# Performance work log

Measured on AMD Instinct MI355X. Metric: run time of the kernel, lower is better.

The kernel has to match this reference:

```python
import jax, jax.numpy as jnp
import numpy as np

B, N, D_IN = 16, 2048, 256
C, H = 32, 64          # num_capsules, dim_capsules
HEADS, KD = 4, 64      # attention heads, key_dim = dim_capsules
ROUTINGS = 3
EPS_SQ = 1e-7
LN_EPS = 1e-3


def squash(v, axis=-1):
    s2 = jnp.sum(jnp.square(v), axis=axis, keepdims=True)
    scale = s2 / (1.0 + s2) / jnp.sqrt(s2 + EPS_SQ)
    return scale * v


def setup_inputs() -> dict:
    key = jax.random.key(0)
    ks = jax.random.split(key, 10)
    # VarianceScaling(scale=2.0, fan_avg, uniform) for W
    fan_avg = (D_IN + H) / 2.0
    limit = float(np.sqrt(3.0 * 2.0 / fan_avg))
    W = jax.random.uniform(ks[0], (C, D_IN, H), minval=-limit, maxval=limit, dtype=jnp.float32)
    b_caps = jnp.zeros((C, H), jnp.float32)
    gamma = jnp.full((1,), 3.0, jnp.float32)
    x = jax.random.normal(ks[1], (B, N, D_IN), dtype=jnp.float32)
    def glorot(k, shape):
        fin, fout = shape[0], int(np.prod(shape[1:]))
        lim = float(np.sqrt(6.0 / (fin + fout)))
        return jax.random.uniform(k, shape, minval=-lim, maxval=lim, dtype=jnp.float32)
    Wq = glorot(ks[2], (H, HEADS, KD)); bq = jnp.zeros((HEADS, KD), jnp.float32)
    Wk = glorot(ks[3], (H, HEADS, KD)); bk = jnp.zeros((HEADS, KD), jnp.float32)
    Wv = glorot(ks[4], (H, HEADS, KD)); bv = jnp.zeros((HEADS, KD), jnp.float32)
    Wo = glorot(ks[5], (HEADS, KD, H)); bo = jnp.zeros((H,), jnp.float32)
    ln_gamma = jnp.ones((H,), jnp.float32)
    ln_beta = jnp.zeros((H,), jnp.float32)
    return dict(x=x, W=W, b_caps=b_caps, gamma=gamma,
                Wq=Wq, bq=bq, Wk=Wk, bk=bk, Wv=Wv, bv=bv, Wo=Wo, bo=bo,
                ln_gamma=ln_gamma, ln_beta=ln_beta)


def dynamic_routing(u_hat):
    # u_hat: [B, N, C, H]
    b = jnp.zeros(u_hat.shape[:3] + (1,), u_hat.dtype)
    v = None
    for i in range(ROUTINGS):
        c = jax.nn.softmax(b, axis=2)                      # [B,N,C,1]
        s = jnp.sum(c * u_hat, axis=1, keepdims=True)      # [B,1,C,H]
        v = squash(s, axis=-1)
        if i < ROUTINGS - 1:
            agreement = jnp.sum(u_hat * v, axis=-1, keepdims=True)
            b = b + agreement
    return jnp.squeeze(v, axis=1)                          # [B,C,H]


def mha_self(xq, Wq, bq, Wk, bk, Wv, bv, Wo, bo):
    # xq: [B, C, H]
    q = jnp.einsum('bch,hnk->bcnk', xq, Wq) + bq
    k = jnp.einsum('bch,hnk->bcnk', xq, Wk) + bk
    v = jnp.einsum('bch,hnk->bcnk', xq, Wv) + bv
    scores = jnp.einsum('bqnd,bknd->bnqk', q, k) / jnp.sqrt(jnp.asarray(KD, xq.dtype))
    attn = jax.nn.softmax(scores, axis=-1)
    ctx = jnp.einsum('bnqk,bknd->bqnd', attn, v)
    return jnp.einsum('bqnd,ndh->bqh', ctx, Wo) + bo


def reference(x, W, b_caps, gamma, Wq, bq, Wk, bk, Wv, bv, Wo, bo, ln_gamma, ln_beta):
    u_hat = jnp.einsum('bnd,cdh->bnch', x, W) + b_caps[None, None]  # [B,N,C,H]
    routed = dynamic_routing(u_hat)                                  # [B,C,H]
    attended = mha_self(routed, Wq, bq, Wk, bk, Wv, bv, Wo, bo)
    y = attended + routed
    mu = jnp.mean(y, axis=-1, keepdims=True)
    var = jnp.mean(jnp.square(y - mu), axis=-1, keepdims=True)
    routed = (y - mu) / jnp.sqrt(var + LN_EPS) * ln_gamma + ln_beta
    return squash(routed, axis=-1) * gamma
```

## Files before the change

### kernel.cpp

```cpp
#include <hip/hip_runtime.h>
#include <cstddef>

typedef _Float16 f16;
typedef __attribute__((ext_vector_type(8))) _Float16 f16x8;
typedef __attribute__((ext_vector_type(4))) float f32x4;

namespace {
constexpr int kB = 16;
constexpr int kN = 2048;
constexpr int kD = 256;
constexpr int kC = 32;
constexpr int kH = 64;
constexpr int kHeads = 4;
constexpr int kKD = 64;
constexpr int kChunks = 32;
constexpr int kRows = kN / kChunks;
constexpr int kXJ = 64;

constexpr size_t OFF_XPART = 0;
constexpr size_t OFF_V     = OFF_XPART + 262144;
constexpr size_t OFF_WV    = OFF_V + 32768;
constexpr size_t OFF_BV    = OFF_WV + 131072;
constexpr size_t OFF_Y     = OFF_BV + 512;
constexpr size_t OFF_CS    = OFF_Y + 131072;
constexpr size_t OFF_QKV   = OFF_CS + 512;
constexpr size_t OFF_CTX   = OFF_QKV + 393216;
constexpr size_t OFF_XF16  = OFF_CTX + 524288;
constexpr size_t OFF_WVH   = OFF_XF16 + 4194304;
constexpr size_t OFF_CSP   = OFF_WVH + 65536;
constexpr size_t OFF_YP    = OFF_CSP + 16384;
constexpr size_t WS_NEED_PARTIAL = (OFF_YP + 4194304) * sizeof(float);
}

__global__ __launch_bounds__(256) void k_xpart(const float* __restrict__ x,
                                               float* __restrict__ xpart,
                                               f16* __restrict__ xh) {
  const int b = blockIdx.x, j = blockIdx.y, d = threadIdx.x;
  const size_t base = ((size_t)b * kN + (size_t)j * 32) * kD + d;
  const float* xp = x + base;
  f16* xo = xh + base;
  float s = 0.f;
#pragma unroll
  for (int n = 0; n < 32; ++n) {
    const float v = xp[(size_t)n * kD];
    s += v;
    xo[(size_t)n * kD] = (f16)v;
  }
  xpart[((size_t)b * kXJ + j) * kD + d] = s;
}

__global__ __launch_bounds__(256) void k_sv(
    const float* __restrict__ W, const float* __restrict__ b_caps,
    const float* __restrict__ xpart, const float* __restrict__ y,
    const float* __restrict__ csum, const float* __restrict__ ypart,
    const float* __restrict__ cspart, float* __restrict__ v,
    float* __restrict__ Wv, f16* __restrict__ Wvh, float* __restrict__ bv,
    const int mode, const int computeWv, const int accWv, const int npart) {
  const int bc = blockIdx.x, b = bc >> 5, c = bc & 31;
  const int t = threadIdx.x;
  const int w = t >> 6, h = t & 63;
  __shared__ float yL[kD];
  __shared__ float sL[4][kH];
  __shared__ float vL[kH];
  __shared__ float csLs;

  if (mode == 0) {
    float s = 0.f;
#pragma unroll 8
    for (int j = 0; j < kXJ; ++j) s += xpart[((size_t)b * kXJ + j) * kD + t];
    yL[t] = s * (1.f / (float)kC);
    if (t == 0) csLs = (float)kN / (float)kC;
  } else if (npart > 0) {
    float s = 0.f;
#pragma unroll 8
    for (int ch = 0; ch < kChunks; ++ch)
      s += ypart[(((size_t)b * kChunks + ch) * kC + c) * kD + t];
    yL[t] = s;
    if (t < 32) {
      float cs_ = cspart[((size_t)b * kChunks + t) * kC + c];
#pragma unroll
      for (int off = 16; off; off >>= 1) cs_ += __shfl_xor(cs_, off, 64);
      if (t == 0) csLs = cs_;
    }
  } else {
    yL[t] = y[(size_t)bc * kD + t];
    if (t == 0) csLs = csum[bc];
  }
  __syncthreads();

  const float* Wc = W + (size_t)c * kD * kH;
  {
    float acc = 0.f;
#pragma unroll 8
    for (int d = w * 64; d < (w + 1) * 64; ++d)
      acc = fmaf(yL[d], Wc[(size_t)d * kH + h], acc);
    sL[w][h] = acc;
  }
  __syncthreads();

  if (t < 64) {
    const float bch = b_caps[c * kH + h];
    float s = sL[0][h] + sL[1][h] + sL[2][h] + sL[3][h] + csLs * bch;
    float s2 = s * s;
#pragma unroll
    for (int off = 32; off; off >>= 1) s2 += __shfl_xor(s2, off, 64);
    const float scale = s2 / (1.f + s2) * rsqrtf(s2 + 1e-7f);
    const float vh = scale * s;
    v[(size_t)bc * kH + h] = vh;
    vL[h] = vh;
    if (computeWv) {
      float bvp = bch * vh;
#pragma unroll
      for (int off = 32; off; off >>= 1) bvp += __shfl_xor(bvp, off, 64);
      if (h == 0) bv[bc] = accWv ? (bv[bc] + bvp) : bvp;
    }
  }
  __syncthreads();
  if (computeWv) {
    float acc = 0.f;
    const float* Wrow = Wc + (size_t)t * kH;
#pragma unroll 8
    for (int hh = 0; hh < kH; ++hh) acc = fmaf(Wrow[hh], vL[hh], acc);
    const size_t idx = (size_t)bc * kD + t;
    const float nv = accWv ? (Wv[idx] + acc) : acc;
    Wv[idx] = nv;
    Wvh[idx] = (f16)nv;
  }
}

__global__ __launch_bounds__(256) void k_route(
    const f16* __restrict__ xh, const f16* __restrict__ Wvh,
    const float* __restrict__ bv, float* __restrict__ y,
    float* __restrict__ csum, float* __restrict__ ypart,
    float* __restrict__ cspart, const int usePart) {
  const int b = blockIdx.x, chunk = blockIdx.y;
  const int t = threadIdx.x;
  const int lane = t & 63, w = t >> 6;
  const int l15 = lane & 15, q = lane >> 4;

  __shared__ __align__(16) f16 xsT[kD][kRows + 8];
  __shared__ float aL[kRows][kC + 4];
  __shared__ __align__(16) f16 pT[kC][kRows + 8];
  __shared__ float csL[8][kC];

  const int n0 = chunk * kRows;
  const float bvc = bv[b * kC + (t & 31)];

  f32x4 acc0 = {0.f, 0.f, 0.f, 0.f}, acc1 = {0.f, 0.f, 0.f, 0.f};
  {
    const int row = w * 16 + l15;
    const f16x8* Ar = reinterpret_cast<const f16x8*>(
        xh + ((size_t)(b * kN + n0 + row)) * kD + q * 8);
    const f16x8* B0 = reinterpret_cast<const f16x8*>(
        Wvh + ((size_t)(b * kC + l15)) * kD + q * 8);
    const f16x8* B1 = reinterpret_cast<const f16x8*>(
        Wvh + ((size_t)(b * kC + 16 + l15)) * kD + q * 8);
#pragma unroll
    for (int ks = 0; ks < 8; ++ks) {
      f16x8 af = Ar[ks * 4];
      acc0 = __builtin_amdgcn_mfma_f32_16x16x32_f16(af, B0[ks * 4], acc0, 0, 0, 0);
      acc1 = __builtin_amdgcn_mfma_f32_16x16x32_f16(af, B1[ks * 4], acc1, 0, 0, 0);
      const int dbase = ks * 32 + q * 8;
#pragma unroll
      for (int i = 0; i < 8; ++i) {
        const int ii = (i + 2 * q) & 7;
        xsT[dbase + ii][row] = af[ii];
      }
    }
  }
#pragma unroll
  for (int r = 0; r < 4; ++r) {
    aL[w * 16 + q * 4 + r][l15] = acc0[r];
    aL[w * 16 + q * 4 + r][16 + l15] = acc1[r];
  }
  __syncthreads();

  const int c = t & 31, sg = t >> 5;
  float csreg = 0.f;
#pragma unroll
  for (int k = 0; k < 8; ++k) {
    const int r = sg * 8 + k;
    float L = bvc + aL[r][c];
    float m = L;
#pragma unroll
    for (int off = 16; off; off >>= 1) m = fmaxf(m, __shfl_xor(m, off, 64));
    const float e = __expf(L - m);
    float ssum = e;
#pragma unroll
    for (int off = 16; off; off >>= 1) ssum += __shfl_xor(ssum, off, 64);
    const float p = e / ssum;
    pT[c][r] = (f16)p;
    csreg += p;
  }
  csL[sg][c] = csreg;
  __syncthreads();

  const int mt2 = w & 1;
  const int ntb = (w >> 1) * 8;
  const f16x8 a0 = *reinterpret_cast<const f16x8*>(&pT[mt2 * 16 + l15][q * 8]);
  const f16x8 a1 = *reinterpret_cast<const f16x8*>(&pT[mt2 * 16 + l15][32 + q * 8]);
  const int cap = mt2 * 16 + q * 4;
#pragma unroll
  for (int i = 0; i < 8; ++i) {
    const int d0 = (ntb + i) * 16;
    const f16x8 b0 = *reinterpret_cast<const f16x8*>(&xsT[d0 + l15][q * 8]);
    const f16x8 b1 = *reinterpret_cast<const f16x8*>(&xsT[d0 + l15][32 + q * 8]);
    f32x4 o = {0.f, 0.f, 0.f, 0.f};
    o = __builtin_amdgcn_mfma_f32_16x16x32_f16(a0, b0, o, 0, 0, 0);
    o = __builtin_amdgcn_mfma_f32_16x16x32_f16(a1, b1, o, 0, 0, 0);
    if (usePart) {
      float* dst = ypart + (((size_t)(b * kChunks + chunk)) * kC + cap) * kD + d0 + l15;
#pragma unroll
      for (int r = 0; r < 4; ++r) dst[(size_t)r * kD] = o[r];
    } else {
      float* dst = y + ((size_t)(b * kC + cap)) * kD + d0 + l15;
#pragma unroll
      for (int r = 0; r < 4; ++r) atomicAdd(dst + (size_t)r * kD, o[r]);
    }
  }
  if (t < 32) {
    float s = 0.f;
#pragma unroll
    for (int j = 0; j < 8; ++j) s += csL[j][t];
    if (usePart) cspart[((size_t)b * kChunks + chunk) * kC + t] = s;
    else atomicAdd(csum + b * kC + t, s);
  }
}

__global__ __launch_bounds__(256) void k_qkv(
    const float* __restrict__ routed, const float* __restrict__ Wq,
    const float* __restrict__ bq, const float* __restrict__ Wk,
    const float* __restrict__ bk, const float* __restrict__ Wvp,
    const float* __restrict__ bvp, float* __restrict__ qkv) {
  const int b = blockIdx.x, head = blockIdx.y, which = blockIdx.z;
  const int t = threadIdx.x;
  const int kk = t & 63, w = t >> 6;
  const float* Wsrc = (which == 0) ? Wq : (which == 1) ? Wk : Wvp;
  const float* bsrc = (which == 0) ? bq : (which == 1) ? bk : bvp;
  __shared__ float rL[kC * kH];
#pragma unroll
  for (int i = 0; i < 8; ++i) rL[t + 256 * i] = routed[(size_t)b * kC * kH + t + 256 * i];
  __syncthreads();
  float acc[8];
  const float bb = bsrc[head * kKD + kk];
#pragma unroll
  for (int i = 0; i < 8; ++i) acc[i] = bb;
#pragma unroll 4
  for (int hh = 0; hh < kH; ++hh) {
    const float wv = Wsrc[((size_t)hh * kHeads + head) * kKD + kk];
#pragma unroll
    for (int i = 0; i < 8; ++i)
      acc[i] = fmaf(rL[(w + 4 * i) * kH + hh], wv, acc[i]);
  }
#pragma unroll
  for (int i = 0; i < 8; ++i) {
    const int cc = w + 4 * i;
    qkv[((((size_t)which * kB + b) * kHeads + head) * kC + cc) * kKD + kk] = acc[i];
  }
}

__global__ __launch_bounds__(256) void k_attn2(const float* __restrict__ qkv,
                                               float* __restrict__ ctx) {
  const int b = blockIdx.x, head = blockIdx.y, t = threadIdx.x;
  constexpr size_t kWhichStride = (size_t)kB * kHeads * kC * kKD;
  const size_t base = ((size_t)b * kHeads + head) * kC * kKD;
  __shared__ float qL[kC][kKD];
  __shared__ float kL[kC][kKD + 1];
  __shared__ float vL[kC][kKD];
  __shared__ float sc[kC][kC + 1];
#pragma unroll
  for (int i = 0; i < 8; ++i) {
    const int e = t + 256 * i, cc = e >> 6, kk = e & 63;
    qL[cc][kk] = qkv[base + e];
    kL[cc][kk] = qkv[base + kWhichStride + e];
    vL[cc][kk] = qkv[base + 2 * kWhichStride + e];
  }
  __syncthreads();
#pragma unroll
  for (int i = 0; i < 4; ++i) {
    const int e = t + 256 * i, qc = e >> 5, kc = e & 31;
    float s = 0.f;
#pragma unroll 8
    for (int d = 0; d < kKD; ++d) s = fmaf(qL[qc][d], kL[kc][d], s);
    sc[qc][kc] = s * 0.125f;
  }
  __syncthreads();
  if (t < kC) {
    float m = -1e30f;
#pragma unroll
    for (int kc = 0; kc < kC; ++kc) m = fmaxf(m, sc[t][kc]);
    float ssum = 0.f;
#pragma unroll
    for (int kc = 0; kc < kC; ++kc) {
      const float e2 = __expf(sc[t][kc] - m);
      sc[t][kc] = e2;
      ssum += e2;
    }
    const float inv = 1.f / ssum;
#pragma unroll
    for (int kc = 0; kc < kC; ++kc) sc[t][kc] *= inv;
  }
  __syncthreads();
#pragma unroll
  for (int i = 0; i < 8; ++i) {
    const int e = t + 256 * i, qc = e >> 6, d = e & 63;
    float s = 0.f;
#pragma unroll 8
    for (int kc = 0; kc < kC; ++kc) s = fmaf(sc[qc][kc], vL[kc][d], s);
    ctx[(((size_t)b * kC + qc) * kHeads + head) * kKD + d] = s;
  }
}

__global__ __launch_bounds__(256) void k_final(
    const float* __restrict__ ctx, const float* __restrict__ Wo,
    const float* __restrict__ bo, const float* __restrict__ routed,
    const float* __restrict__ ln_g, const float* __restrict__ ln_b,
    const float* __restrict__ gamma, float* __restrict__ out) {
  const int bc = blockIdx.x, t = threadIdx.x;
  const int w = t >> 6, h = t & 63;
  __shared__ float cL[kHeads * kKD];
  __shared__ float sL[4][kH];
  cL[t] = ctx[(size_t)bc * (kHeads * kKD) + t];
  __syncthreads();
  float acc = 0.f;
#pragma unroll 8
  for (int nd = w * 64; nd < (w + 1) * 64; ++nd)
    acc = fmaf(cL[nd], Wo[(size_t)nd * kH + h], acc);
  sL[w][h] = acc;
  __syncthreads();
  if (t < 64) {
    const float yv = sL[0][h] + sL[1][h] + sL[2][h] + sL[3][h] + bo[h] +
                     routed[(size_t)bc * kH + h];
    float mu = yv;
#pragma unroll
    for (int off = 32; off; off >>= 1) mu += __shfl_xor(mu, off, 64);
    mu *= (1.f / (float)kH);
    const float dv = yv - mu;
    float var = dv * dv;
#pragma unroll
    for (int off = 32; off; off >>= 1) var += __shfl_xor(var, off, 64);
    var *= (1.f / (float)kH);
    const float nrm = dv * rsqrtf(var + 1e-3f) * ln_g[h] + ln_b[h];
    float s2 = nrm * nrm;
#pragma unroll
    for (int off = 32; off; off >>= 1) s2 += __shfl_xor(s2, off, 64);
    const float scale = s2 / (1.f + s2) * rsqrtf(s2 + 1e-7f);
    out[(size_t)bc * kH + h] = scale * nrm * gamma[0];
  }
}

extern "C" void kernel_launch(void* const* d_in, const int* in_sizes, int n_in,
                              void* d_out, int out_size, void* d_ws, size_t ws_size,
                              hipStream_t stream) {
  (void)in_sizes; (void)n_in; (void)out_size;
  const float* x      = (const float*)d_in[0];
  const float* W      = (const float*)d_in[1];
  const float* b_caps = (const float*)d_in[2];
  const float* gamma  = (const float*)d_in[3];
  const float* Wq     = (const float*)d_in[4];
  const float* bq     = (const float*)d_in[5];
  const float* Wk     = (const float*)d_in[6];
  const float* bk     = (const float*)d_in[7];
  const float* Wv_in  = (const float*)d_in[8];
  const float* bv_in  = (const float*)d_in[9];
  const float* Wo     = (const float*)d_in[10];
  const float* bo     = (const float*)d_in[11];
  const float* ln_g   = (const float*)d_in[12];
  const float* ln_b   = (const float*)d_in[13];
  float* out = (float*)d_out;
  float* ws  = (float*)d_ws;

  float* xpart = ws + OFF_XPART;
  float* v     = ws + OFF_V;
  float* Wv    = ws + OFF_WV;
  float* bv    = ws + OFF_BV;
  float* y     = ws + OFF_Y;
  float* cs    = ws + OFF_CS;
  float* qkv   = ws + OFF_QKV;
  float* ctx   = ws + OFF_CTX;
  f16*   xf16  = (f16*)(ws + OFF_XF16);
  f16*   wvh   = (f16*)(ws + OFF_WVH);
  float* csp   = ws + OFF_CSP;
  float* yp    = ws + OFF_YP;

  const int usePart = (ws_size >= WS_NEED_PARTIAL) ? 1 : 0;

  k_xpart<<<dim3(kB, kXJ), 256, 0, stream>>>(x, xpart, xf16);
  k_sv<<<kB * kC, 256, 0, stream>>>(W, b_caps, xpart, y, cs, yp, csp, v, Wv, wvh, bv,
                                    0, 1, 0, 0);

  if (!usePart) {
    hipMemsetAsync(y, 0, (size_t)kB * kC * kD * sizeof(float), stream);
    hipMemsetAsync(cs, 0, (size_t)kB * kC * sizeof(float), stream);
  }
  k_route<<<dim3(kB, kChunks), 256, 0, stream>>>(xf16, wvh, bv, y, cs, yp, csp, usePart);
  k_sv<<<kB * kC, 256, 0, stream>>>(W, b_caps, xpart, y, cs, yp, csp, v, Wv, wvh, bv,
                                    1, 1, 1,
                                    usePart ? kChunks : 0);

  if (!usePart) {
    hipMemsetAsync(y, 0, (size_t)kB * kC * kD * sizeof(float), stream);
    hipMemsetAsync(cs, 0, (size_t)kB * kC * sizeof(float), stream);
  }
  k_route<<<dim3(kB, kChunks), 256, 0, stream>>>(xf16, wvh, bv, y, cs, yp, csp, usePart);
  k_sv<<<kB * kC, 256, 0, stream>>>(W, b_caps, xpart, y, cs, yp, csp, v, Wv, wvh, bv,
                                    1, 0, 0,
                                    usePart ? kChunks : 0);

  k_qkv<<<dim3(kB, kHeads, 3), 256, 0, stream>>>(v, Wq, bq, Wk, bk, Wv_in, bv_in, qkv);
  k_attn2<<<dim3(kB, kHeads), 256, 0, stream>>>(qkv, ctx);
  k_final<<<kB * kC, 256, 0, stream>>>(ctx, Wo, bo, v, ln_g, ln_b, gamma, out);
}
```

Baseline: 179.0 us.

## Fuse final squash, QKV, attention and output projection into one per-batch kernel

```diff
diff --git a/kernel.cpp b/kernel.cpp
--- a/kernel.cpp
+++ b/kernel.cpp
@@ -2,6 +2,7 @@
 #include <cstddef>
 
 typedef _Float16 f16;
+typedef __attribute__((ext_vector_type(4))) _Float16 f16x4;
 typedef __attribute__((ext_vector_type(8))) _Float16 f16x8;
 typedef __attribute__((ext_vector_type(4))) float f32x4;
 
@@ -23,9 +24,7 @@
 constexpr size_t OFF_BV    = OFF_WV + 131072;
 constexpr size_t OFF_Y     = OFF_BV + 512;
 constexpr size_t OFF_CS    = OFF_Y + 131072;
-constexpr size_t OFF_QKV   = OFF_CS + 512;
-constexpr size_t OFF_CTX   = OFF_QKV + 393216;
-constexpr size_t OFF_XF16  = OFF_CTX + 524288;
+constexpr size_t OFF_XF16  = OFF_CS + 512;
 constexpr size_t OFF_WVH   = OFF_XF16 + 4194304;
 constexpr size_t OFF_CSP   = OFF_WVH + 65536;
 constexpr size_t OFF_YP    = OFF_CSP + 16384;
@@ -35,18 +34,25 @@
 __global__ __launch_bounds__(256) void k_xpart(const float* __restrict__ x,
                                                float* __restrict__ xpart,
                                                f16* __restrict__ xh) {
-  const int b = blockIdx.x, j = blockIdx.y, d = threadIdx.x;
-  const size_t base = ((size_t)b * kN + (size_t)j * 32) * kD + d;
-  const float* xp = x + base;
-  f16* xo = xh + base;
-  float s = 0.f;
-#pragma unroll
-  for (int n = 0; n < 32; ++n) {
-    const float v = xp[(size_t)n * kD];
-    s += v;
-    xo[(size_t)n * kD] = (f16)v;
-  }
-  xpart[((size_t)b * kXJ + j) * kD + d] = s;
+  const int b = blockIdx.x, j = blockIdx.y;
+  const int t = threadIdx.x;
+  const int rg = t >> 6, dq = t & 63;
+  __shared__ float sL[4][kD];
+  float4 s = {0.f, 0.f, 0.f, 0.f};
+  const size_t rowbase = (size_t)b * kN + (size_t)j * 32;
+#pragma unroll
+  for (int i = 0; i < 8; ++i) {
+    const int r = rg * 8 + i;
+    const float4 q = *(reinterpret_cast<const float4*>(x + (rowbase + r) * kD) + dq);
+    s.x += q.x; s.y += q.y; s.z += q.z; s.w += q.w;
+    f16x4 h4 = {(f16)q.x, (f16)q.y, (f16)q.z, (f16)q.w};
+    *(reinterpret_cast<f16x4*>(xh + (rowbase + r) * kD) + dq) = h4;
+  }
+  reinterpret_cast<float4*>(&sL[rg][0])[dq] = s;
+  __syncthreads();
+  const int d = t;
+  xpart[((size_t)b * kXJ + j) * kD + d] =
+      sL[0][d] + sL[1][d] + sL[2][d] + sL[3][d];
 }
 
 __global__ __launch_bounds__(256) void k_sv(
@@ -227,125 +233,181 @@
   }
 }
 
-__global__ __launch_bounds__(256) void k_qkv(
-    const float* __restrict__ routed, const float* __restrict__ Wq,
-    const float* __restrict__ bq, const float* __restrict__ Wk,
-    const float* __restrict__ bk, const float* __restrict__ Wvp,
-    const float* __restrict__ bvp, float* __restrict__ qkv) {
-  const int b = blockIdx.x, head = blockIdx.y, which = blockIdx.z;
-  const int t = threadIdx.x;
-  const int kk = t & 63, w = t >> 6;
-  const float* Wsrc = (which == 0) ? Wq : (which == 1) ? Wk : Wvp;
-  const float* bsrc = (which == 0) ? bq : (which == 1) ? bk : bvp;
-  __shared__ float rL[kC * kH];
-#pragma unroll
-  for (int i = 0; i < 8; ++i) rL[t + 256 * i] = routed[(size_t)b * kC * kH + t + 256 * i];
-  __syncthreads();
-  float acc[8];
-  const float bb = bsrc[head * kKD + kk];
-#pragma unroll
-  for (int i = 0; i < 8; ++i) acc[i] = bb;
+__global__ __launch_bounds__(256) void k_tail(
+    const float* __restrict__ W, const float* __restrict__ b_caps,
+    const float* __restrict__ y, const float* __restrict__ csum,
+    const float* __restrict__ ypart, const float* __restrict__ cspart,
+    const float* __restrict__ Wq, const float* __restrict__ bq,
+    const float* __restrict__ Wk, const float* __restrict__ bk,
+    const float* __restrict__ Wvp, const float* __restrict__ bvp,
+    const float* __restrict__ Wo, const float* __restrict__ bo,
+    const float* __restrict__ ln_g, const float* __restrict__ ln_b,
+    const float* __restrict__ gamma, float* __restrict__ out,
+    const int usePart) {
+  const int b = blockIdx.x, t = threadIdx.x;
+  const int w = t >> 6, h = t & 63;
+  __shared__ float yL[kC][kD];
+  __shared__ float rL[kC][kH];
+  __shared__ float csLs[kC];
+  __shared__ float qLs[kC][kKD];
+  __shared__ float kLs[kC][kKD + 1];
+  __shared__ float vLs[kC][kKD];
+  __shared__ float scs[kC][kC + 1];
+
+  if (usePart) {
+    const int c = t >> 3, fq = t & 7;
+    float4 acc[8];
+#pragma unroll
+    for (int i = 0; i < 8; ++i) acc[i] = {0.f, 0.f, 0.f, 0.f};
+    for (int ch = 0; ch < kChunks; ++ch) {
+      const float4* src = reinterpret_cast<const float4*>(
+          ypart + (((size_t)(b * kChunks + ch)) * kC + c) * kD);
+#pragma unroll
+      for (int i = 0; i < 8; ++i) {
+        const float4 q = src[fq + 8 * i];
+        acc[i].x += q.x; acc[i].y += q.y; acc[i].z += q.z; acc[i].w += q.w;
+      }
+    }
+    float4* dst = reinterpret_cast<float4*>(&yL[c][0]);
+#pragma unroll
+    for (int i = 0; i < 8; ++i) dst[fq + 8 * i] = acc[i];
+    if (t < kC) {
+      float s = 0.f;
+      for (int ch = 0; ch < kChunks; ++ch)
+        s += cspart[((size_t)b * kChunks + ch) * kC + t];
+      csLs[t] = s;
+    }
+  } else {
+    const int c = t >> 3, fq = t & 7;
+    const float4* src = reinterpret_cast<const float4*>(y + ((size_t)(b * kC + c)) * kD);
+    float4* dst = reinterpret_cast<float4*>(&yL[c][0]);
+#pragma unroll
+    for (int i = 0; i < 8; ++i) dst[fq + 8 * i] = src[fq + 8 * i];
+    if (t < kC) csLs[t] = csum[b * kC + t];
+  }
+  __syncthreads();
+
+  {
+    float sacc[8];
+#pragma unroll
+    for (int i = 0; i < 8; ++i) {
+      const int c = w + 4 * i;
+      sacc[i] = csLs[c] * b_caps[c * kH + h];
+    }
+#pragma unroll
+    for (int i = 0; i < 8; ++i) {
+      const int c = w + 4 * i;
+      const float* Wc = W + ((size_t)c * kD) * kH + h;
+      float a = sacc[i];
+#pragma unroll 8
+      for (int d = 0; d < kD; ++d) a = fmaf(yL[c][d], Wc[(size_t)d * kH], a);
+      sacc[i] = a;
+    }
+#pragma unroll
+    for (int i = 0; i < 8; ++i) {
+      const int c = w + 4 * i;
+      float s2 = sacc[i] * sacc[i];
+#pragma unroll
+      for (int off = 32; off; off >>= 1) s2 += __shfl_xor(s2, off, 64);
+      const float scale = s2 / (1.f + s2) * rsqrtf(s2 + 1e-7f);
+      rL[c][h] = scale * sacc[i];
+    }
+  }
+  __syncthreads();
+
+  for (int head = 0; head < kHeads; ++head) {
+    float aq[8], ak[8], av[8];
+    const float bq_ = bq[head * kKD + h];
+    const float bk_ = bk[head * kKD + h];
+    const float bv_ = bvp[head * kKD + h];
+#pragma unroll
+    for (int i = 0; i < 8; ++i) { aq[i] = bq_; ak[i] = bk_; av[i] = bv_; }
 #pragma unroll 4
-  for (int hh = 0; hh < kH; ++hh) {
-    const float wv = Wsrc[((size_t)hh * kHeads + head) * kKD + kk];
-#pragma unroll
-    for (int i = 0; i < 8; ++i)
-      acc[i] = fmaf(rL[(w + 4 * i) * kH + hh], wv, acc[i]);
-  }
-#pragma unroll
-  for (int i = 0; i < 8; ++i) {
-    const int cc = w + 4 * i;
-    qkv[((((size_t)which * kB + b) * kHeads + head) * kC + cc) * kKD + kk] = acc[i];
-  }
-}
-
-__global__ __launch_bounds__(256) void k_attn2(const float* __restrict__ qkv,
-                                               float* __restrict__ ctx) {
-  const int b = blockIdx.x, head = blockIdx.y, t = threadIdx.x;
-  constexpr size_t kWhichStride = (size_t)kB * kHeads * kC * kKD;
-  const size_t base = ((size_t)b * kHeads + head) * kC * kKD;
-  __shared__ float qL[kC][kKD];
-  __shared__ float kL[kC][kKD + 1];
-  __shared__ float vL[kC][kKD];
-  __shared__ float sc[kC][kC + 1];
-#pragma unroll
-  for (int i = 0; i < 8; ++i) {
-    const int e = t + 256 * i, cc = e >> 6, kk = e & 63;
-    qL[cc][kk] = qkv[base + e];
-    kL[cc][kk] = qkv[base + kWhichStride + e];
-    vL[cc][kk] = qkv[base + 2 * kWhichStride + e];
-  }
-  __syncthreads();
-#pragma unroll
-  for (int i = 0; i < 4; ++i) {
-    const int e = t + 256 * i, qc = e >> 5, kc = e & 31;
-    float s = 0.f;
-#pragma unroll 8
-    for (int d = 0; d < kKD; ++d) s = fmaf(qL[qc][d], kL[kc][d], s);
-    sc[qc][kc] = s * 0.125f;
-  }
-  __syncthreads();
-  if (t < kC) {
-    float m = -1e30f;
-#pragma unroll
-    for (int kc = 0; kc < kC; ++kc) m = fmaxf(m, sc[t][kc]);
-    float ssum = 0.f;
-#pragma unroll
-    for (int kc = 0; kc < kC; ++kc) {
-      const float e2 = __expf(sc[t][kc] - m);
-      sc[t][kc] = e2;
-      ssum += e2;
-    }
-    const float inv = 1.f / ssum;
-#pragma unroll
-    for (int kc = 0; kc < kC; ++kc) sc[t][kc] *= inv;
-  }
-  __syncthreads();
-#pragma unroll
-  for (int i = 0; i < 8; ++i) {
-    const int e = t + 256 * i, qc = e >> 6, d = e & 63;
-    float s = 0.f;
-#pragma unroll 8
-    for (int kc = 0; kc < kC; ++kc) s = fmaf(sc[qc][kc], vL[kc][d], s);
-    ctx[(((size_t)b * kC + qc) * kHeads + head) * kKD + d] = s;
-  }
-}
-
-__global__ __launch_bounds__(256) void k_final(
-    const float* __restrict__ ctx, const float* __restrict__ Wo,
-    const float* __restrict__ bo, const float* __restrict__ routed,
-    const float* __restrict__ ln_g, const float* __restrict__ ln_b,
-    const float* __restrict__ gamma, float* __restrict__ out) {
-  const int bc = blockIdx.x, t = threadIdx.x;
-  const int w = t >> 6, h = t & 63;
-  __shared__ float cL[kHeads * kKD];
-  __shared__ float sL[4][kH];
-  cL[t] = ctx[(size_t)bc * (kHeads * kKD) + t];
-  __syncthreads();
-  float acc = 0.f;
-#pragma unroll 8
-  for (int nd = w * 64; nd < (w + 1) * 64; ++nd)
-    acc = fmaf(cL[nd], Wo[(size_t)nd * kH + h], acc);
-  sL[w][h] = acc;
-  __syncthreads();
-  if (t < 64) {
-    const float yv = sL[0][h] + sL[1][h] + sL[2][h] + sL[3][h] + bo[h] +
-                     routed[(size_t)bc * kH + h];
-    float mu = yv;
-#pragma unroll
-    for (int off = 32; off; off >>= 1) mu += __shfl_xor(mu, off, 64);
-    mu *= (1.f / (float)kH);
-    const float dv = yv - mu;
-    float var = dv * dv;
-#pragma unroll
-    for (int off = 32; off; off >>= 1) var += __shfl_xor(var, off, 64);
-    var *= (1.f / (float)kH);
-    const float nrm = dv * rsqrtf(var + 1e-3f) * ln_g[h] + ln_b[h];
-    float s2 = nrm * nrm;
-#pragma unroll
-    for (int off = 32; off; off >>= 1) s2 += __shfl_xor(s2, off, 64);
-    const float scale = s2 / (1.f + s2) * rsqrtf(s2 + 1e-7f);
-    out[(size_t)bc * kH + h] = scale * nrm * gamma[0];
+    for (int hh = 0; hh < kH; ++hh) {
+      const size_t wi = ((size_t)hh * kHeads + head) * kKD + h;
+      const float wq = Wq[wi], wk = Wk[wi], wv2 = Wvp[wi];
+#pragma unroll
+      for (int i = 0; i < 8; ++i) {
+        const float r = rL[w + 4 * i][hh];
+        aq[i] = fmaf(r, wq, aq[i]);
+        ak[i] = fmaf(r, wk, ak[i]);
+        av[i] = fmaf(r, wv2, av[i]);
+      }
+    }
+#pragma unroll
+    for (int i = 0; i < 8; ++i) {
+      const int c = w + 4 * i;
+      qLs[c][h] = aq[i]; kLs[c][h] = ak[i]; vLs[c][h] = av[i];
+    }
+    __syncthreads();
+#pragma unroll
+    for (int i2 = 0; i2 < 4; ++i2) {
+      const int e = t + 256 * i2, qc = e >> 5, kc = e & 31;
+      float s = 0.f;
+#pragma unroll 8
+      for (int d = 0; d < kKD; ++d) s = fmaf(qLs[qc][d], kLs[kc][d], s);
+      scs[qc][kc] = s * 0.125f;
+    }
+    __syncthreads();
+    if (t < kC) {
+      float m = -1e30f;
+#pragma unroll
+      for (int kc = 0; kc < kC; ++kc) m = fmaxf(m, scs[t][kc]);
+      float ssum = 0.f;
+#pragma unroll
+      for (int kc = 0; kc < kC; ++kc) {
+        const float e2 = __expf(scs[t][kc] - m);
+        scs[t][kc] = e2;
+        ssum += e2;
+      }
+      const float inv = 1.f / ssum;
+#pragma unroll
+      for (int kc = 0; kc < kC; ++kc) scs[t][kc] *= inv;
+    }
+    __syncthreads();
+#pragma unroll
+    for (int i2 = 0; i2 < 8; ++i2) {
+      const int e = t + 256 * i2, qc = e >> 6, d = e & 63;
+      float s = 0.f;
+#pragma unroll 8
+      for (int kc = 0; kc < kC; ++kc) s = fmaf(scs[qc][kc], vLs[kc][d], s);
+      yL[qc][head * kKD + d] = s;
+    }
+    __syncthreads();
+  }
+
+  {
+    float accO[8];
+    const float bo_ = bo[h];
+#pragma unroll
+    for (int i = 0; i < 8; ++i) accO[i] = bo_;
+#pragma unroll 4
+    for (int nd = 0; nd < kHeads * kKD; ++nd) {
+      const float wo = Wo[(size_t)nd * kH + h];
+#pragma unroll
+      for (int i = 0; i < 8; ++i) accO[i] = fmaf(yL[w + 4 * i][nd], wo, accO[i]);
+    }
+    const float lg = ln_g[h], lb = ln_b[h], g0 = gamma[0];
+#pragma unroll
+    for (int i = 0; i < 8; ++i) {
+      const int c = w + 4 * i;
+      const float yv = accO[i] + rL[c][h];
+      float mu = yv;
+#pragma unroll
+      for (int off = 32; off; off >>= 1) mu += __shfl_xor(mu, off, 64);
+      mu *= (1.f / (float)kH);
+      const float dv = yv - mu;
+      float var = dv * dv;
+#pragma unroll
+      for (int off = 32; off; off >>= 1) var += __shfl_xor(var, off, 64);
+      var *= (1.f / (float)kH);
+      const float nrm = dv * rsqrtf(var + 1e-3f) * lg + lb;
+      float s2 = nrm * nrm;
+#pragma unroll
+      for (int off = 32; off; off >>= 1) s2 += __shfl_xor(s2, off, 64);
+      const float scale = s2 / (1.f + s2) * rsqrtf(s2 + 1e-7f);
+      out[((size_t)b * kC + c) * kH + h] = scale * nrm * g0;
+    }
   }
 }
 
@@ -376,8 +438,6 @@
   float* bv    = ws + OFF_BV;
   float* y     = ws + OFF_Y;
   float* cs    = ws + OFF_CS;
-  float* qkv   = ws + OFF_QKV;
-  float* ctx   = ws + OFF_CTX;
   f16*   xf16  = (f16*)(ws + OFF_XF16);
   f16*   wvh   = (f16*)(ws + OFF_WVH);
   float* csp   = ws + OFF_CSP;
@@ -403,11 +463,8 @@
     hipMemsetAsync(cs, 0, (size_t)kB * kC * sizeof(float), stream);
   }
   k_route<<<dim3(kB, kChunks), 256, 0, stream>>>(xf16, wvh, bv, y, cs, yp, csp, usePart);
-  k_sv<<<kB * kC, 256, 0, stream>>>(W, b_caps, xpart, y, cs, yp, csp, v, Wv, wvh, bv,
-                                    1, 0, 0,
-                                    usePart ? kChunks : 0);
-
-  k_qkv<<<dim3(kB, kHeads, 3), 256, 0, stream>>>(v, Wq, bq, Wk, bk, Wv_in, bv_in, qkv);
-  k_attn2<<<dim3(kB, kHeads), 256, 0, stream>>>(qkv, ctx);
-  k_final<<<kB * kC, 256, 0, stream>>>(ctx, Wo, bo, v, ln_g, ln_b, gamma, out);
-}
+
+  k_tail<<<kB, 256, 0, stream>>>(W, b_caps, y, cs, yp, csp,
+                                 Wq, bq, Wk, bk, Wv_in, bv_in, Wo, bo,
+                                 ln_g, ln_b, gamma, out, usePart);
+}
```

Result: slower. 308.5 us (+72.3%).
